# Optimization experiments

Measured on AMD Instinct MI355X. Metric: run time of the kernel, lower is better.

Reference implementation:

```python
import jax, jax.numpy as jnp
import numpy as np

N_NODES = 100000
N_EDGES = 1600000
N_GRAPHS = 256


def setup_inputs() -> dict:
    key = jax.random.key(0)
    ks = jax.random.split(key, 7)
    x = jax.random.normal(ks[0], (N_NODES, 128), dtype=jnp.float32)
    W1 = jax.random.normal(ks[1], (128, 64), dtype=jnp.float32) * (1.0 / np.sqrt(128))
    W2 = jax.random.normal(ks[2], (64, 64), dtype=jnp.float32) * (1.0 / np.sqrt(64))
    W3 = jax.random.normal(ks[3], (64, 64), dtype=jnp.float32) * (1.0 / np.sqrt(64))
    Wlin = jax.random.normal(ks[4], (64, 16), dtype=jnp.float32) * (1.0 / np.sqrt(64))
    edge_index = jax.random.randint(ks[5], (2, N_EDGES), 0, N_NODES, dtype=jnp.int64)
    batch = jnp.sort(jax.random.randint(ks[6], (N_NODES,), 0, N_GRAPHS, dtype=jnp.int64))
    return {"x": x, "W1": W1, "W2": W2, "W3": W3, "Wlin": Wlin,
            "edge_index": edge_index, "batch": batch}


def _gcn_conv(h, W, src, dst):
    # GCNConv(bias=False, normalize=False): scatter-add of transformed src feats onto dst
    m = h @ W                                   # [N, d_out]
    return jax.ops.segment_sum(m[src], dst, num_segments=N_NODES)


def reference(x, W1, W2, W3, Wlin, edge_index, batch):
    src, dst = edge_index[0], edge_index[1]
    h = jax.nn.relu(_gcn_conv(x, W1, src, dst))
    h = jax.nn.relu(_gcn_conv(h, W2, src, dst))
    h = _gcn_conv(h, W3, src, dst)
    # global mean pool over graphs
    sums = jax.ops.segment_sum(h, batch, num_segments=N_GRAPHS)      # [G, d]
    counts = jax.ops.segment_sum(jnp.ones((N_NODES,), h.dtype), batch,
                                 num_segments=N_GRAPHS)              # [G]
    pooled = sums / jnp.maximum(counts, 1.0)[:, None]
    return pooled @ Wlin                                             # [G, out]
```

## Files before the change

kernel.cpp:

```cpp
#include <hip/hip_runtime.h>
#include <hip/hip_bf16.h>

#define SCAN_CHUNK 1024
#define BIN_CHUNK  4096
#define BSH        9
#define BCAP       10240
#define GSLOTS     16
#define KNODES     2

typedef __attribute__((ext_vector_type(8))) short short8v;
typedef __attribute__((ext_vector_type(4))) float f32x4;

__device__ __forceinline__ unsigned short f2bf(float f) {
    union { float f; unsigned int i; } c;
    c.f = f;
    unsigned int r = c.i + 0x7FFFu + ((c.i >> 16) & 1u);
    return (unsigned short)(r >> 16);
}
__device__ __forceinline__ float lo2f(unsigned int u) {
    union { unsigned int i; float f; } c; c.i = u << 16; return c.f;
}
__device__ __forceinline__ float hi2f(unsigned int u) {
    union { unsigned int i; float f; } c; c.i = u & 0xFFFF0000u; return c.f;
}
__device__ __forceinline__ unsigned int pack2bf(float lo, float hi) {
    return ((unsigned int)f2bf(hi) << 16) | (unsigned int)f2bf(lo);
}
__device__ __forceinline__ int idx_at(const void* p, long long i, int is64) {
    if (is64) return (int)((const long long*)p)[i];
    return ((const int*)p)[i];
}
__device__ __forceinline__ short8v as_s8(uint4 q) {
    return __builtin_bit_cast(short8v, q);
}

__global__ __launch_bounds__(256) void k_setup(const unsigned int* __restrict__ a, long long aWords,
                                               const unsigned int* __restrict__ b, long long bWords,
                                               int* __restrict__ flags, int* __restrict__ bcur,
                                               float* __restrict__ T, int tN,
                                               const float* __restrict__ W1, const float* __restrict__ W2,
                                               const float* __restrict__ W3, const float* __restrict__ Wlin,
                                               float* __restrict__ Wc,
                                               unsigned short* __restrict__ Wt1hi, unsigned short* __restrict__ Wt1lo,
                                               unsigned short* __restrict__ Wt2hi, unsigned short* __restrict__ Wt2lo) {
    int t = threadIdx.x;
    if (blockIdx.x == 0) {
        __shared__ int sA, sB;
        if (t == 0) { sA = 1; sB = 1; }
        __syncthreads();
        long long hA = aWords / 2;
        long long pA = 2 * ((long long)t * (hA - 1) / 255) + 1;
        if (a[pA] != 0u) atomicAnd(&sA, 0);
        long long hB = bWords / 2;
        long long pB = 2 * ((long long)t * (hB - 1) / 255) + 1;
        if (b[pB] != 0u) atomicAnd(&sB, 0);
        __syncthreads();
        if (t == 0) { flags[0] = sA; flags[1] = sB; }
    } else if (blockIdx.x == 1) {
        bcur[t] = 0;
        for (int o = t; o < 64 * 16; o += 256) {
            int k = o >> 4, j = o & 15;
            float acc = 0.f;
#pragma unroll 8
            for (int m = 0; m < 64; ++m) acc += W3[k * 64 + m] * Wlin[m * 16 + j];
            Wc[o] = acc;
        }
    } else if (blockIdx.x == 2) {
        int col = t >> 2, ks = (t & 3) * 32;
        for (int k = ks; k < ks + 32; ++k) {
            float v = W1[(size_t)k * 64 + col];
            unsigned short h = f2bf(v);
            Wt1hi[col * 128 + k] = h;
            Wt1lo[col * 128 + k] = f2bf(v - lo2f(h));
        }
    } else if (blockIdx.x == 3) {
        int col = t >> 2, ks = (t & 3) * 16;
        for (int k = ks; k < ks + 16; ++k) {
            float v = W2[(size_t)k * 64 + col];
            unsigned short h = f2bf(v);
            Wt2hi[col * 64 + k] = h;
            Wt2lo[col * 64 + k] = f2bf(v - lo2f(h));
        }
    } else {
        int i = (blockIdx.x - 4) * 256 + t;
        if (i < tN) T[i] = 0.f;
    }
}

__global__ __launch_bounds__(256) void k_bin(const void* __restrict__ ei, int nE,
                                             int* __restrict__ bcur, unsigned int* __restrict__ srcsE,
                                             const int* __restrict__ flags) {
    __shared__ int eS[BIN_CHUNK], eD[BIN_CHUNK];
    __shared__ int cntD[256], baseD[256], posD[256];
    int t = threadIdx.x;
    int is64 = flags[0];
    cntD[t] = 0; posD[t] = 0;
    __syncthreads();
    int cs = blockIdx.x * BIN_CHUNK;
    int ce = min(cs + BIN_CHUNK, nE);
    for (int i = cs + t; i < ce; i += 256) {
        int src = idx_at(ei, i, is64);
        int dst = idx_at(ei, (long long)nE + i, is64);
        eS[i - cs] = src; eD[i - cs] = dst;
        atomicAdd(&cntD[dst >> BSH], 1);
    }
    __syncthreads();
    if (cntD[t] > 0) baseD[t] = atomicAdd(&bcur[t], cntD[t]);
    __syncthreads();
    for (int i = cs + t; i < ce; i += 256) {
        int src = eS[i - cs], dst = eD[i - cs];
        int kd = dst >> BSH;
        int od = baseD[kd] + atomicAdd(&posD[kd], 1);
        if (od < BCAP)
            srcsE[(size_t)kd * BCAP + od] = (unsigned int)src | ((unsigned int)(dst & 511) << 17);
    }
}

__global__ __launch_bounds__(256) void k_fill3(unsigned int* __restrict__ srcsE,
                                               const int* __restrict__ bcur,
                                               int* __restrict__ rowstart, int* __restrict__ rowend,
                                               int N) {
    __shared__ unsigned int ent[BCAP];
    __shared__ int cnt5[512], off5[512], cur5[512], s2[256];
    int k = blockIdx.x;
    int t = threadIdx.x;
    int base = k * BCAP;
    int ck = min(bcur[k], BCAP);
    cnt5[t] = 0; cnt5[t + 256] = 0;
    __syncthreads();
    for (int i = t; i < ck; i += 256) {
        unsigned int v = srcsE[base + i];
        ent[i] = v;
        atomicAdd(&cnt5[v >> 17], 1);
    }
    __syncthreads();
    int pair = cnt5[2 * t] + cnt5[2 * t + 1];
    s2[t] = pair;
    __syncthreads();
    for (int off = 1; off < 256; off <<= 1) {
        int x = (t >= off) ? s2[t - off] : 0;
        __syncthreads();
        s2[t] += x;
        __syncthreads();
    }
    int excl = s2[t] - pair;
    off5[2 * t] = excl;
    off5[2 * t + 1] = excl + cnt5[2 * t];
    __syncthreads();
    for (int j = t; j < 512; j += 256) {
        int node = (k << BSH) + j;
        if (node < N) {
            rowstart[node] = base + off5[j];
            rowend[node]   = base + off5[j] + cnt5[j];
        }
        cur5[j] = off5[j];
    }
    __syncthreads();
    for (int i = t; i < ck; i += 256) {
        unsigned int v = ent[i];
        int d = (int)(v >> 17);
        int pos = atomicAdd(&cur5[d], 1);
        srcsE[base + pos] = v & 0x1FFFFu;
    }
}

__global__ __launch_bounds__(256) void k_zero_i(int* __restrict__ p, int n) {
    int i = blockIdx.x * 256 + threadIdx.x;
    if (i < n) p[i] = 0;
}
__global__ __launch_bounds__(256) void k_hist(const void* __restrict__ ei, int nE,
                                              int* __restrict__ cnt, const int* __restrict__ flags) {
    int e = blockIdx.x * 256 + threadIdx.x;
    if (e >= nE) return;
    int is64 = flags[0];
    atomicAdd(&cnt[idx_at(ei, (long long)nE + e, is64)], 1);
}
__global__ __launch_bounds__(256) void k_scan_a(const int* __restrict__ cnt, int N, int* __restrict__ bsum) {
    __shared__ int s[256];
    int b = blockIdx.x, t = threadIdx.x;
    int base = b * SCAN_CHUNK + t * 4;
    int v = 0;
#pragma unroll
    for (int j = 0; j < 4; ++j) if (base + j < N) v += cnt[base + j];
    s[t] = v; __syncthreads();
    for (int off = 128; off >= 1; off >>= 1) {
        if (t < off) s[t] += s[t + off];
        __syncthreads();
    }
    if (t == 0) bsum[b] = s[0];
}
__global__ __launch_bounds__(128) void k_scan_b(const int* __restrict__ bsum, int NB, int* __restrict__ bpre) {
    __shared__ int s[128];
    int t = threadIdx.x;
    int v = (t < NB) ? bsum[t] : 0;
    s[t] = v; __syncthreads();
    for (int off = 1; off < 128; off <<= 1) {
        int x = (t >= off) ? s[t - off] : 0;
        __syncthreads();
        s[t] += x;
        __syncthreads();
    }
    if (t < NB) bpre[t] = s[t] - v;
}
__global__ __launch_bounds__(256) void k_scan_c(const int* __restrict__ cnt, int N,
                                                const int* __restrict__ bpre,
                                                int* __restrict__ rowstart, int* __restrict__ rowend,
                                                int* __restrict__ cursor) {
    __shared__ int s[256];
    int b = blockIdx.x, t = threadIdx.x;
    int base = b * SCAN_CHUNK + t * 4;
    int c0 = (base + 0 < N) ? cnt[base + 0] : 0;
    int c1 = (base + 1 < N) ? cnt[base + 1] : 0;
    int c2 = (base + 2 < N) ? cnt[base + 2] : 0;
    int c3 = (base + 3 < N) ? cnt[base + 3] : 0;
    int p0 = c0, p1 = p0 + c1, p2 = p1 + c2, p3 = p2 + c3;
    s[t] = p3; __syncthreads();
    int tot = p3;
    for (int off = 1; off < 256; off <<= 1) {
        int x = (t >= off) ? s[t - off] : 0;
        __syncthreads();
        s[t] += x;
        __syncthreads();
    }
    int toff = s[t] - tot + bpre[b];
    if (base + 0 < N) { rowstart[base + 0] = toff;      rowend[base + 0] = toff + p0; cursor[base + 0] = toff; }
    if (base + 1 < N) { rowstart[base + 1] = toff + p0; rowend[base + 1] = toff + p1; cursor[base + 1] = toff + p0; }
    if (base + 2 < N) { rowstart[base + 2] = toff + p1; rowend[base + 2] = toff + p2; cursor[base + 2] = toff + p1; }
    if (base + 3 < N) { rowstart[base + 3] = toff + p2; rowend[base + 3] = toff + p3; cursor[base + 3] = toff + p2; }
}
__global__ __launch_bounds__(256) void k_fill(const void* __restrict__ ei, int nE,
                                              int* __restrict__ cursor, int* __restrict__ srcs,
                                              const int* __restrict__ flags) {
    int e = blockIdx.x * 256 + threadIdx.x;
    if (e >= nE) return;
    int is64 = flags[0];
    int src = idx_at(ei, e, is64);
    int dst = idx_at(ei, (long long)nE + e, is64);
    int pos = atomicAdd(&cursor[dst], 1);
    srcs[pos] = src;
}

__global__ __launch_bounds__(256) void k_gemm1m(const float* __restrict__ X,
                                                const unsigned short* __restrict__ Wthi,
                                                const unsigned short* __restrict__ Wtlo,
                                                unsigned short* __restrict__ Mb, int N) {
    __shared__ unsigned short Xhi[64 * 128];
    __shared__ unsigned short Xlo[64 * 128];
    int tid = threadIdx.x;
    int wid = tid >> 6, lane = tid & 63;
    int lrow = lane & 15, lk = lane >> 4;
    int base = blockIdx.x * 64;

    uint4 bhi[4], blo[4];
    {
        int col = wid * 16 + lrow;
        const unsigned short* ph = Wthi + col * 128 + lk * 8;
        const unsigned short* pl = Wtlo + col * 128 + lk * 8;
#pragma unroll
        for (int kc = 0; kc < 4; ++kc) {
            bhi[kc] = *(const uint4*)(ph + kc * 32);
            blo[kc] = *(const uint4*)(pl + kc * 32);
        }
    }

    {
        int r = tid >> 2, seg = tid & 3;
        int row = base + r;
        float v[32];
        if (row < N) {
            const float4* src = (const float4*)(X + (size_t)row * 128 + seg * 32);
#pragma unroll
            for (int u = 0; u < 8; ++u) {
                float4 f = src[u];
                v[4 * u] = f.x; v[4 * u + 1] = f.y; v[4 * u + 2] = f.z; v[4 * u + 3] = f.w;
            }
        } else {
#pragma unroll
            for (int u = 0; u < 32; ++u) v[u] = 0.f;
        }
        int swz = (r & 7) << 4;
#pragma unroll
        for (int u = 0; u < 4; ++u) {
            unsigned short h[8];
            float lo[8];
#pragma unroll
            for (int j = 0; j < 8; ++j) {
                float xv = v[u * 8 + j];
                unsigned short hh = f2bf(xv);
                h[j] = hh;
                lo[j] = xv - lo2f(hh);
            }
            uint4 qh, ql;
            qh.x = ((unsigned)h[1] << 16) | h[0]; qh.y = ((unsigned)h[3] << 16) | h[2];
            qh.z = ((unsigned)h[5] << 16) | h[4]; qh.w = ((unsigned)h[7] << 16) | h[6];
            ql.x = pack2bf(lo[0], lo[1]); ql.y = pack2bf(lo[2], lo[3]);
            ql.z = pack2bf(lo[4], lo[5]); ql.w = pack2bf(lo[6], lo[7]);
            int kb = seg * 64 + u * 16;
            int addr = r * 256 + (kb ^ swz);
            *(uint4*)((char*)Xhi + addr) = qh;
            *(uint4*)((char*)Xlo + addr) = ql;
        }
    }
    __syncthreads();

    int col = wid * 16 + lrow;
#pragma unroll
    for (int rt = 0; rt < 4; ++rt) {
        f32x4 acc = {0.f, 0.f, 0.f, 0.f};
        int row = rt * 16 + lrow;
        int rbase = row * 256;
        int swz = (row & 7) << 4;
#pragma unroll
        for (int kc = 0; kc < 4; ++kc) {
            int kb = kc * 64 + lk * 16;
            uint4 ah = *(const uint4*)((const char*)Xhi + rbase + (kb ^ swz));
            uint4 al = *(const uint4*)((const char*)Xlo + rbase + (kb ^ swz));
            acc = __builtin_amdgcn_mfma_f32_16x16x32_bf16(as_s8(ah), as_s8(bhi[kc]), acc, 0, 0, 0);
            acc = __builtin_amdgcn_mfma_f32_16x16x32_bf16(as_s8(al), as_s8(bhi[kc]), acc, 0, 0, 0);
            acc = __builtin_amdgcn_mfma_f32_16x16x32_bf16(as_s8(ah), as_s8(blo[kc]), acc, 0, 0, 0);
        }
#pragma unroll
        for (int j = 0; j < 4; ++j) {
            int orow = base + rt * 16 + lk * 4 + j;
            if (orow < N) Mb[(size_t)orow * 64 + col] = f2bf(acc[j]);
        }
    }
}

__global__ __launch_bounds__(256) void k_projm(const unsigned short* __restrict__ Rb,
                                               const unsigned short* __restrict__ Wthi,
                                               const unsigned short* __restrict__ Wtlo,
                                               unsigned short* __restrict__ Mout, int N) {
    __shared__ unsigned short Rs[64 * 64];
    int tid = threadIdx.x;
    int wid = tid >> 6, lane = tid & 63;
    int lrow = lane & 15, lk = lane >> 4;
    int base = blockIdx.x * 64;

    uint4 bhi[2], blo[2];
    {
        int col = wid * 16 + lrow;
        const unsigned short* ph = Wthi + col * 64 + lk * 8;
        const unsigned short* pl = Wtlo + col * 64 + lk * 8;
#pragma unroll
        for (int kc = 0; kc < 2; ++kc) {
            bhi[kc] = *(const uint4*)(ph + kc * 32);
            blo[kc] = *(const uint4*)(pl + kc * 32);
        }
    }
    {
        int r = tid >> 2, seg = tid & 3;
        int row = base + r;
        uint4 q0, q1;
        if (row < N) {
            const uint4* src = (const uint4*)(Rb + (size_t)row * 64 + seg * 16);
            q0 = src[0]; q1 = src[1];
        } else {
            q0 = make_uint4(0u, 0u, 0u, 0u); q1 = q0;
        }
        int swz = (r & 7) << 4;
        int kb = seg * 32;
        *(uint4*)((char*)Rs + r * 128 + ((kb) ^ swz)) = q0;
        *(uint4*)((char*)Rs + r * 128 + ((kb + 16) ^ swz)) = q1;
    }
    __syncthreads();

    int col = wid * 16 + lrow;
#pragma unroll
    for (int rt = 0; rt < 4; ++rt) {
        f32x4 acc = {0.f, 0.f, 0.f, 0.f};
        int row = rt * 16 + lrow;
        int rbase = row * 128;
        int swz = (row & 7) << 4;
#pragma unroll
        for (int kc = 0; kc < 2; ++kc) {
            int kb = kc * 64 + lk * 16;
            uint4 a = *(const uint4*)((const char*)Rs + rbase + (kb ^ swz));
            acc = __builtin_amdgcn_mfma_f32_16x16x32_bf16(as_s8(a), as_s8(bhi[kc]), acc, 0, 0, 0);
            acc = __builtin_amdgcn_mfma_f32_16x16x32_bf16(as_s8(a), as_s8(blo[kc]), acc, 0, 0, 0);
        }
#pragma unroll
        for (int j = 0; j < 4; ++j) {
            int orow = base + rt * 16 + lk * 4 + j;
            if (orow < N) Mout[(size_t)orow * 64 + col] = f2bf(acc[j]);
        }
    }
}

#define GATHER8_CORE(SRCS, MB, S, E, LMASK, L, A)                             \
    {                                                                         \
        int c_ = (S);                                                         \
        for (; c_ + 8 <= (E); c_ += 8) {                                      \
            int sv_ = (SRCS)[c_ + (L)];                                       \
            _Pragma("unroll")                                                 \
            for (int j_ = 0; j_ < 8; ++j_) {                                  \
                int srcn_ = __shfl(sv_, (LMASK) | j_, 64);                    \
                uint4 p_ = ((const uint4*)((MB) + (size_t)srcn_ * 64))[L];    \
                A[0] += lo2f(p_.x); A[1] += hi2f(p_.x);                       \
                A[2] += lo2f(p_.y); A[3] += hi2f(p_.y);                       \
                A[4] += lo2f(p_.z); A[5] += hi2f(p_.z);                       \
                A[6] += lo2f(p_.w); A[7] += hi2f(p_.w);                       \
            }                                                                 \
        }                                                                     \
        if (c_ < (E)) {                                                       \
            int sv_ = (SRCS)[(c_ + (L) < (E)) ? c_ + (L) : (E) - 1];          \
            _Pragma("unroll")                                                 \
            for (int j_ = 0; j_ < 8; ++j_) {                                  \
                if (c_ + j_ < (E)) {                                          \
                    int srcn_ = __shfl(sv_, (LMASK) | j_, 64);                \
                    uint4 p_ = ((const uint4*)((MB) + (size_t)srcn_ * 64))[L];\
                    A[0] += lo2f(p_.x); A[1] += hi2f(p_.x);                   \
                    A[2] += lo2f(p_.y); A[3] += hi2f(p_.y);                   \
                    A[4] += lo2f(p_.z); A[5] += hi2f(p_.z);                   \
                    A[6] += lo2f(p_.w); A[7] += hi2f(p_.w);                   \
                }                                                             \
            }                                                                 \
        }                                                                     \
    }

__global__ __launch_bounds__(256) void k_gather8(const unsigned short* __restrict__ Mb,
                                                 const int* __restrict__ rowstart,
                                                 const int* __restrict__ rowend,
                                                 const int* __restrict__ srcs,
                                                 unsigned short* __restrict__ R, int N) {
    int tid = threadIdx.x;
    int lane = tid & 63;
    int l = lane & 7;
    int lmask = lane & 56;
    int node0 = (blockIdx.x * 32 + (tid >> 3)) * KNODES;
#pragma unroll
    for (int jn = 0; jn < KNODES; ++jn) {
        int node = node0 + jn;
        if (node >= N) break;
        int s = rowstart[node], e = rowend[node];
        float a[8] = {0.f, 0.f, 0.f, 0.f, 0.f, 0.f, 0.f, 0.f};
        GATHER8_CORE(srcs, Mb, s, e, lmask, l, a)
        uint4 q;
        q.x = pack2bf(fmaxf(a[0], 0.f), fmaxf(a[1], 0.f));
        q.y = pack2bf(fmaxf(a[2], 0.f), fmaxf(a[3], 0.f));
        q.z = pack2bf(fmaxf(a[4], 0.f), fmaxf(a[5], 0.f));
        q.w = pack2bf(fmaxf(a[6], 0.f), fmaxf(a[7], 0.f));
        ((uint4*)(R + (size_t)node * 64))[l] = q;
    }
}

#define GFLUSH(GG, RR)                                                        \
    {                                                                         \
        int slot_ = (GG) - gmin;                                              \
        if (slot_ >= 0 && slot_ < GSLOTS) {                                   \
            _Pragma("unroll")                                                 \
            for (int i_ = 0; i_ < 8; ++i_)                                    \
                atomicAdd(&sacc[slot_][l * 8 + i_], RR[i_]);                  \
        } else {                                                              \
            _Pragma("unroll")                                                 \
            for (int i_ = 0; i_ < 8; ++i_)                                    \
                atomicAdd(&T[(GG) * 64 + l * 8 + i_], RR[i_]);                \
        }                                                                     \
    }

__global__ __launch_bounds__(256) void k_gsum8(const unsigned short* __restrict__ R,
                                               const int* __restrict__ rowstart,
                                               const int* __restrict__ rowend,
                                               const int* __restrict__ srcs,
                                               const void* __restrict__ batch,
                                               float* __restrict__ T, int N, int G,
                                               const int* __restrict__ flags) {
    __shared__ float sacc[GSLOTS][64];
    int tid = threadIdx.x;
    for (int t = tid; t < GSLOTS * 64; t += 256) ((float*)sacc)[t] = 0.f;
    int is64 = flags[1];
    int nbase = blockIdx.x * 32 * KNODES;
    int gmin = idx_at(batch, min(nbase, N - 1), is64);
    __syncthreads();

    int lane = tid & 63;
    int l = lane & 7;
    int lmask = lane & 56;
    int node0 = nbase + (tid >> 3) * KNODES;
    float r[8] = {0.f, 0.f, 0.f, 0.f, 0.f, 0.f, 0.f, 0.f};
    int curG = -1;
#pragma unroll
    for (int jn = 0; jn < KNODES; ++jn) {
        int node = node0 + jn;
        if (node >= N) break;
        int s = rowstart[node], e = rowend[node];
        float a[8] = {0.f, 0.f, 0.f, 0.f, 0.f, 0.f, 0.f, 0.f};
        GATHER8_CORE(srcs, R, s, e, lmask, l, a)
        int g = idx_at(batch, node, is64);
        if (g != curG) {
            if (curG >= 0) GFLUSH(curG, r)
#pragma unroll
            for (int i = 0; i < 8; ++i) r[i] = a[i];
            curG = g;
        } else {
#pragma unroll
            for (int i = 0; i < 8; ++i) r[i] += a[i];
        }
    }
    if (curG >= 0) GFLUSH(curG, r)
    __syncthreads();
    for (int t = tid; t < GSLOTS * 64; t += 256) {
        float v = ((float*)sacc)[t];
        int g = gmin + (t >> 6);
        if (v != 0.f && g < G) atomicAdd(&T[g * 64 + (t & 63)], v);
    }
}

__global__ __launch_bounds__(64) void k_out(const float* __restrict__ T,
                                            const void* __restrict__ batch,
                                            const float* __restrict__ Wc,
                                            float* __restrict__ out, int N,
                                            const int* __restrict__ flags) {
    int g = blockIdx.x;
    int lane = threadIdx.x;
    int is64 = flags[1];

    int lo = 0, hi = N;
    while (lo < hi) { int mid = (lo + hi) >> 1; if (idx_at(batch, mid, is64) < g) lo = mid + 1; else hi = mid; }
    int s = lo;
    lo = s; hi = N;
    while (lo < hi) { int mid = (lo + hi) >> 1; if (idx_at(batch, mid, is64) < g + 1) lo = mid + 1; else hi = mid; }
    float cnt = (float)(lo - s);

    __shared__ float P[64];
    P[lane] = T[g * 64 + lane] / fmaxf(cnt, 1.0f);
    __syncthreads();
    if (lane < 16) {
        float o = 0.f;
#pragma unroll 8
        for (int k = 0; k < 64; ++k) o += P[k] * Wc[k * 16 + lane];
        out[g * 16 + lane] = o;
    }
}

extern "C" void kernel_launch(void* const* d_in, const int* in_sizes, int n_in,
                              void* d_out, int out_size, void* d_ws, size_t ws_size,
                              hipStream_t stream) {
    const float* x    = (const float*)d_in[0];
    const float* W1   = (const float*)d_in[1];
    const float* W2   = (const float*)d_in[2];
    const float* W3   = (const float*)d_in[3];
    const float* Wlin = (const float*)d_in[4];
    const void* ei    = d_in[5];
    const void* batch = d_in[6];

    int N  = in_sizes[0] / 128;
    int nE = in_sizes[5] / 2;
    int G  = out_size / 16;
    int NBUCK = (N + (1 << BSH) - 1) >> BSH;
    int NB = (N + SCAN_CHUNK - 1) / SCAN_CHUNK;
    bool fast = (NBUCK <= 256);

    unsigned short* MbA = (unsigned short*)d_ws;
    unsigned short* MbB = (unsigned short*)(MbA + (size_t)N * 64);
    int* ip       = (int*)(MbB + (size_t)N * 64);
    int* rowstart = ip;          ip += N;
    int* rowend   = ip;          ip += N;
    int* cnt      = ip;          ip += N;
    int* bsum     = ip;          ip += 128;
    int* bpre     = ip;          ip += 128;
    int* flags    = ip;          ip += 2;
    int* bcur     = ip;          ip += 256;
    float* T      = (float*)ip;  ip += (size_t)G * 64;
    float* Wc     = (float*)ip;  ip += 64 * 16;
    unsigned short* Wt1hi = (unsigned short*)ip; ip += 4096;
    unsigned short* Wt1lo = (unsigned short*)ip; ip += 4096;
    unsigned short* Wt2hi = (unsigned short*)ip; ip += 2048;
    unsigned short* Wt2lo = (unsigned short*)ip; ip += 2048;
    unsigned int* srcsE = (unsigned int*)ip;
    ip += fast ? (size_t)256 * BCAP : (size_t)nE;
    size_t need = (size_t)((char*)ip - (char*)d_ws);
    if (ws_size < need) return;

    dim3 blk(256);
    int gT64  = (N + 63) / 64;
    int gG8   = (N + 32 * KNODES - 1) / (32 * KNODES);
    int gBin  = (nE + BIN_CHUNK - 1) / BIN_CHUNK;
    int tN    = G * 64;
    int gSetup = 4 + (tN + 255) / 256;

    hipLaunchKernelGGL(k_setup, dim3(gSetup), blk, 0, stream,
                       (const unsigned int*)ei, (long long)in_sizes[5],
                       (const unsigned int*)batch, (long long)in_sizes[6],
                       flags, bcur, T, tN, W1, W2, W3, Wlin, Wc,
                       Wt1hi, Wt1lo, Wt2hi, Wt2lo);

    if (fast) {
        hipLaunchKernelGGL(k_bin,   dim3(gBin), blk, 0, stream, ei, nE, bcur, srcsE, flags);
        hipLaunchKernelGGL(k_fill3, dim3(NBUCK), blk, 0, stream, srcsE, bcur, rowstart, rowend, N);
    } else {
        int gN = (N + 255) / 256;
        int gE = (nE + 255) / 256;
        hipLaunchKernelGGL(k_zero_i, dim3(gN), blk, 0, stream, cnt, N);
        hipLaunchKernelGGL(k_hist,   dim3(gE), blk, 0, stream, ei, nE, cnt, flags);
        hipLaunchKernelGGL(k_scan_a, dim3(NB), blk, 0, stream, cnt, N, bsum);
        hipLaunchKernelGGL(k_scan_b, dim3(1), dim3(128), 0, stream, bsum, NB, bpre);
        hipLaunchKernelGGL(k_scan_c, dim3(NB), blk, 0, stream, cnt, N, bpre, rowstart, rowend, cnt);
        hipLaunchKernelGGL(k_fill,   dim3(gE), blk, 0, stream, ei, nE, cnt, (int*)srcsE, flags);
    }

    hipLaunchKernelGGL(k_gemm1m,  dim3(gT64), blk, 0, stream, x, Wt1hi, Wt1lo, MbA, N);
    hipLaunchKernelGGL(k_gather8, dim3(gG8), blk, 0, stream, MbA, rowstart, rowend, (const int*)srcsE, MbB, N);
    hipLaunchKernelGGL(k_projm,   dim3(gT64), blk, 0, stream, MbB, Wt2hi, Wt2lo, MbA, N);
    hipLaunchKernelGGL(k_gather8, dim3(gG8), blk, 0, stream, MbA, rowstart, rowend, (const int*)srcsE, MbB, N);
    hipLaunchKernelGGL(k_gsum8, dim3(gG8), blk, 0, stream, MbB, rowstart, rowend, (const int*)srcsE, batch, T, N, G, flags);
    hipLaunchKernelGGL(k_out, dim3(G), dim3(64), 0, stream, T, batch, Wc, (float*)d_out, N, flags);
}
```

Measured before the change: 313.7 us.

## Project layer-3 features through W3·Wlin before final gather-pool to shrink gather width

Moves the combined W3·Wlin projection ahead of the last aggregation: a new MFMA kernel computes 16-wide Y2 = relu(h2)·(W3·Wlin), then a bucket-parallel kernel sums Y2 over edges per graph using graph ids packed into the high bits of the CSR source entries. This cuts the last gather from 64 to 16 bf16 features per edge and drops the final 64x16 matmul. The gather macro is also unrolled to 16 edges per iteration with masking of the packed bits. It adds an extra kernel and relies on graph ids relative to each bucket fitting in 15 bits and on per-bucket graph spans, with a global atomic fallback beyond 32 graph slots.

After: 302.0 us. -3.7%, faster.

```diff
diff --git a/kernel.cpp b/kernel.cpp
--- a/kernel.cpp
+++ b/kernel.cpp
@@ -7,6 +7,8 @@
 #define BCAP       10240
 #define GSLOTS     16
 #define KNODES     2
+#define GS16       32
+#define GSPLIT     2
 
 typedef __attribute__((ext_vector_type(8))) short short8v;
 typedef __attribute__((ext_vector_type(4))) float f32x4;
@@ -42,7 +44,8 @@
                                                const float* __restrict__ W3, const float* __restrict__ Wlin,
                                                float* __restrict__ Wc,
                                                unsigned short* __restrict__ Wt1hi, unsigned short* __restrict__ Wt1lo,
-                                               unsigned short* __restrict__ Wt2hi, unsigned short* __restrict__ Wt2lo) {
+                                               unsigned short* __restrict__ Wt2hi, unsigned short* __restrict__ Wt2lo,
+                                               unsigned short* __restrict__ Wcthi, unsigned short* __restrict__ Wctlo) {
     int t = threadIdx.x;
     if (blockIdx.x == 0) {
         __shared__ int sA, sB;
@@ -64,6 +67,9 @@
 #pragma unroll 8
             for (int m = 0; m < 64; ++m) acc += W3[k * 64 + m] * Wlin[m * 16 + j];
             Wc[o] = acc;
+            unsigned short h = f2bf(acc);
+            Wcthi[j * 64 + k] = h;
+            Wctlo[j * 64 + k] = f2bf(acc - lo2f(h));
         }
     } else if (blockIdx.x == 2) {
         int col = t >> 2, ks = (t & 3) * 32;
@@ -119,14 +125,19 @@
 __global__ __launch_bounds__(256) void k_fill3(unsigned int* __restrict__ srcsE,
                                                const int* __restrict__ bcur,
                                                int* __restrict__ rowstart, int* __restrict__ rowend,
-                                               int N) {
+                                               int N, const void* __restrict__ batch,
+                                               const int* __restrict__ flags) {
     __shared__ unsigned int ent[BCAP];
     __shared__ int cnt5[512], off5[512], cur5[512], s2[256];
+    __shared__ int grelS[512];
+    __shared__ int sgf;
     int k = blockIdx.x;
     int t = threadIdx.x;
     int base = k * BCAP;
     int ck = min(bcur[k], BCAP);
+    int is64b = flags[1];
     cnt5[t] = 0; cnt5[t + 256] = 0;
+    if (t == 0) sgf = idx_at(batch, (long long)(k << BSH), is64b);
     __syncthreads();
     for (int i = t; i < ck; i += 256) {
         unsigned int v = srcsE[base + i];
@@ -152,6 +163,9 @@
         if (node < N) {
             rowstart[node] = base + off5[j];
             rowend[node]   = base + off5[j] + cnt5[j];
+            grelS[j] = idx_at(batch, node, is64b) - sgf;
+        } else {
+            grelS[j] = 0;
         }
         cur5[j] = off5[j];
     }
@@ -160,7 +174,7 @@
         unsigned int v = ent[i];
         int d = (int)(v >> 17);
         int pos = atomicAdd(&cur5[d], 1);
-        srcsE[base + pos] = v & 0x1FFFFu;
+        srcsE[base + pos] = (v & 0x1FFFFu) | ((unsigned int)grelS[d] << 17);
     }
 }
 
@@ -387,32 +401,79 @@
     }
 }
 
-#define GATHER8_CORE(SRCS, MB, S, E, LMASK, L, A)                             \
+__global__ __launch_bounds__(256) void k_y2(const unsigned short* __restrict__ R,
+                                            const unsigned short* __restrict__ Wcthi,
+                                            const unsigned short* __restrict__ Wctlo,
+                                            unsigned short* __restrict__ Y2, int N) {
+    int tid = threadIdx.x;
+    int wid = tid >> 6, lane = tid & 63;
+    int lrow = lane & 15, lk = lane >> 4;
+    int rowb = blockIdx.x * 64 + wid * 16;
+
+    uint4 bhi[2], blo[2];
+#pragma unroll
+    for (int kc = 0; kc < 2; ++kc) {
+        bhi[kc] = *(const uint4*)(Wcthi + lrow * 64 + kc * 32 + lk * 8);
+        blo[kc] = *(const uint4*)(Wctlo + lrow * 64 + kc * 32 + lk * 8);
+    }
+    f32x4 acc = {0.f, 0.f, 0.f, 0.f};
+    int arow = rowb + lrow;
+#pragma unroll
+    for (int kc = 0; kc < 2; ++kc) {
+        uint4 a = make_uint4(0u, 0u, 0u, 0u);
+        if (arow < N) a = *(const uint4*)(R + (size_t)arow * 64 + kc * 32 + lk * 8);
+        acc = __builtin_amdgcn_mfma_f32_16x16x32_bf16(as_s8(a), as_s8(bhi[kc]), acc, 0, 0, 0);
+        acc = __builtin_amdgcn_mfma_f32_16x16x32_bf16(as_s8(a), as_s8(blo[kc]), acc, 0, 0, 0);
+    }
+#pragma unroll
+    for (int j = 0; j < 4; ++j) {
+        int orow = rowb + lk * 4 + j;
+        if (orow < N) Y2[(size_t)orow * 16 + lrow] = f2bf(acc[j]);
+    }
+}
+
+#define GACC(P)  { A[0] += lo2f((P).x); A[1] += hi2f((P).x);                  \
+                   A[2] += lo2f((P).y); A[3] += hi2f((P).y);                  \
+                   A[4] += lo2f((P).z); A[5] += hi2f((P).z);                  \
+                   A[6] += lo2f((P).w); A[7] += hi2f((P).w); }
+#define GATHER8_CORE(SRCS, MB, S, E, LMASK, L, A, MASK)                       \
     {                                                                         \
         int c_ = (S);                                                         \
-        for (; c_ + 8 <= (E); c_ += 8) {                                      \
-            int sv_ = (SRCS)[c_ + (L)];                                       \
+        for (; c_ + 16 <= (E); c_ += 16) {                                    \
+            int sv0_ = (int)(SRCS)[c_ + (L)];                                 \
+            int sv1_ = (int)(SRCS)[c_ + 8 + (L)];                             \
             _Pragma("unroll")                                                 \
             for (int j_ = 0; j_ < 8; ++j_) {                                  \
-                int srcn_ = __shfl(sv_, (LMASK) | j_, 64);                    \
+                int srcn_ = __shfl(sv0_, (LMASK) | j_, 64) & (int)(MASK);     \
                 uint4 p_ = ((const uint4*)((MB) + (size_t)srcn_ * 64))[L];    \
-                A[0] += lo2f(p_.x); A[1] += hi2f(p_.x);                       \
-                A[2] += lo2f(p_.y); A[3] += hi2f(p_.y);                       \
-                A[4] += lo2f(p_.z); A[5] += hi2f(p_.z);                       \
-                A[6] += lo2f(p_.w); A[7] += hi2f(p_.w);                       \
+                GACC(p_)                                                      \
+            }                                                                 \
+            _Pragma("unroll")                                                 \
+            for (int j_ = 0; j_ < 8; ++j_) {                                  \
+                int srcn_ = __shfl(sv1_, (LMASK) | j_, 64) & (int)(MASK);     \
+                uint4 p_ = ((const uint4*)((MB) + (size_t)srcn_ * 64))[L];    \
+                GACC(p_)                                                      \
             }                                                                 \
         }                                                                     \
-        if (c_ < (E)) {                                                       \
-            int sv_ = (SRCS)[(c_ + (L) < (E)) ? c_ + (L) : (E) - 1];          \
+        if (c_ + 8 <= (E)) {                                                  \
+            int sv_ = (int)(SRCS)[c_ + (L)];                                  \
             _Pragma("unroll")                                                 \
             for (int j_ = 0; j_ < 8; ++j_) {                                  \
-                if (c_ + j_ < (E)) {                                          \
-                    int srcn_ = __shfl(sv_, (LMASK) | j_, 64);                \
+                int srcn_ = __shfl(sv_, (LMASK) | j_, 64) & (int)(MASK);      \
+                uint4 p_ = ((const uint4*)((MB) + (size_t)srcn_ * 64))[L];    \
+                GACC(p_)                                                      \
+            }                                                                 \
+            c_ += 8;                                                          \
+        }                                                                     \
+        if (c_ < (E)) {                                                       \
+            int m_ = (E) - c_;                                                \
+            int sv_ = (int)(SRCS)[(c_ + (L) < (E)) ? c_ + (L) : (E) - 1];     \
+            _Pragma("unroll")                                                 \
+            for (int j_ = 0; j_ < 8; ++j_) {                                  \
+                if (j_ < m_) {                                                \
+                    int srcn_ = __shfl(sv_, (LMASK) | j_, 64) & (int)(MASK);  \
                     uint4 p_ = ((const uint4*)((MB) + (size_t)srcn_ * 64))[L];\
-                    A[0] += lo2f(p_.x); A[1] += hi2f(p_.x);                   \
-                    A[2] += lo2f(p_.y); A[3] += hi2f(p_.y);                   \
-                    A[4] += lo2f(p_.z); A[5] += hi2f(p_.z);                   \
-                    A[6] += lo2f(p_.w); A[7] += hi2f(p_.w);                   \
+                    GACC(p_)                                                  \
                 }                                                             \
             }                                                                 \
         }                                                                     \
@@ -421,8 +482,9 @@
 __global__ __launch_bounds__(256) void k_gather8(const unsigned short* __restrict__ Mb,
                                                  const int* __restrict__ rowstart,
                                                  const int* __restrict__ rowend,
-                                                 const int* __restrict__ srcs,
-                                                 unsigned short* __restrict__ R, int N) {
+                                                 const unsigned int* __restrict__ srcs,
+                                                 unsigned short* __restrict__ R, int N,
+                                                 unsigned int srcMask) {
     int tid = threadIdx.x;
     int lane = tid & 63;
     int l = lane & 7;
@@ -433,15 +495,113 @@
         int node = node0 + jn;
         if (node >= N) break;
         int s = rowstart[node], e = rowend[node];
-        float a[8] = {0.f, 0.f, 0.f, 0.f, 0.f, 0.f, 0.f, 0.f};
-        GATHER8_CORE(srcs, Mb, s, e, lmask, l, a)
+        float A[8] = {0.f, 0.f, 0.f, 0.f, 0.f, 0.f, 0.f, 0.f};
+        GATHER8_CORE(srcs, Mb, s, e, lmask, l, A, srcMask)
         uint4 q;
-        q.x = pack2bf(fmaxf(a[0], 0.f), fmaxf(a[1], 0.f));
-        q.y = pack2bf(fmaxf(a[2], 0.f), fmaxf(a[3], 0.f));
-        q.z = pack2bf(fmaxf(a[4], 0.f), fmaxf(a[5], 0.f));
-        q.w = pack2bf(fmaxf(a[6], 0.f), fmaxf(a[7], 0.f));
+        q.x = pack2bf(fmaxf(A[0], 0.f), fmaxf(A[1], 0.f));
+        q.y = pack2bf(fmaxf(A[2], 0.f), fmaxf(A[3], 0.f));
+        q.z = pack2bf(fmaxf(A[4], 0.f), fmaxf(A[5], 0.f));
+        q.w = pack2bf(fmaxf(A[6], 0.f), fmaxf(A[7], 0.f));
         ((uint4*)(R + (size_t)node * 64))[l] = q;
     }
+}
+
+__global__ __launch_bounds__(256) void k_gsum16(const unsigned short* __restrict__ y2,
+                                                const unsigned int* __restrict__ srcsE,
+                                                const int* __restrict__ bcur,
+                                                const void* __restrict__ batch,
+                                                float* __restrict__ T16, int N, int G,
+                                                const int* __restrict__ flags) {
+    __shared__ float sacc[GS16][4][16];
+    __shared__ int sgmin;
+    int t = threadIdx.x;
+    int k = blockIdx.x / GSPLIT;
+    int half = blockIdx.x % GSPLIT;
+    for (int i = t; i < GS16 * 4 * 16; i += 256) ((float*)sacc)[i] = 0.f;
+    if (t == 0) sgmin = idx_at(batch, (long long)min(k << BSH, N - 1), flags[1]);
+    __syncthreads();
+    int gmin = sgmin;
+    int ck = min(bcur[k], BCAP);
+    int base = k * BCAP;
+    int lo = half * (ck / GSPLIT);
+    int hi = (half == GSPLIT - 1) ? ck : (half + 1) * (ck / GSPLIT);
+    int cnt = hi - lo;
+    int len = (cnt + 255) >> 8;
+    int s0 = lo + t * len;
+    int e0 = min(s0 + len, hi);
+    int rep = t & 3;
+
+    float acc[16];
+#pragma unroll
+    for (int j = 0; j < 16; ++j) acc[j] = 0.f;
+    int curg = -1;
+
+#define GF16(GG)                                                              \
+    {                                                                         \
+        if ((GG) < GS16) {                                                    \
+            float* sp_ = &sacc[GG][rep][0];                                   \
+            _Pragma("unroll")                                                 \
+            for (int j_ = 0; j_ < 16; ++j_) atomicAdd(&sp_[j_], acc[j_]);     \
+        } else {                                                              \
+            _Pragma("unroll")                                                 \
+            for (int j_ = 0; j_ < 16; ++j_)                                   \
+                atomicAdd(&T16[(size_t)(gmin + (GG)) * 16 + j_], acc[j_]);    \
+        }                                                                     \
+    }
+
+    int i = s0;
+    while (i < e0) {
+        if (i + 4 <= e0) {
+            unsigned v0 = srcsE[base + i], v1 = srcsE[base + i + 1];
+            unsigned v2 = srcsE[base + i + 2], v3 = srcsE[base + i + 3];
+            int g0 = (int)(v0 >> 17);
+            if (g0 == curg && (int)(v3 >> 17) == g0 &&
+                (int)(v1 >> 17) == g0 && (int)(v2 >> 17) == g0) {
+                const uint4* p0 = (const uint4*)(y2 + (size_t)(v0 & 0x1FFFFu) * 16);
+                const uint4* p1 = (const uint4*)(y2 + (size_t)(v1 & 0x1FFFFu) * 16);
+                const uint4* p2 = (const uint4*)(y2 + (size_t)(v2 & 0x1FFFFu) * 16);
+                const uint4* p3 = (const uint4*)(y2 + (size_t)(v3 & 0x1FFFFu) * 16);
+                uint4 a0 = p0[0], b0 = p0[1];
+                uint4 a1 = p1[0], b1 = p1[1];
+                uint4 a2 = p2[0], b2 = p2[1];
+                uint4 a3 = p3[0], b3 = p3[1];
+#define Y2ACC(QA, QB)                                                         \
+                acc[0] += lo2f((QA).x); acc[1] += hi2f((QA).x);               \
+                acc[2] += lo2f((QA).y); acc[3] += hi2f((QA).y);               \
+                acc[4] += lo2f((QA).z); acc[5] += hi2f((QA).z);               \
+                acc[6] += lo2f((QA).w); acc[7] += hi2f((QA).w);               \
+                acc[8] += lo2f((QB).x); acc[9] += hi2f((QB).x);               \
+                acc[10] += lo2f((QB).y); acc[11] += hi2f((QB).y);             \
+                acc[12] += lo2f((QB).z); acc[13] += hi2f((QB).z);             \
+                acc[14] += lo2f((QB).w); acc[15] += hi2f((QB).w);
+                Y2ACC(a0, b0) Y2ACC(a1, b1) Y2ACC(a2, b2) Y2ACC(a3, b3)
+                i += 4;
+                continue;
+            }
+        }
+        unsigned v = srcsE[base + i];
+        int g = (int)(v >> 17);
+        if (g != curg) {
+            if (curg >= 0) GF16(curg)
+            curg = g;
+#pragma unroll
+            for (int j = 0; j < 16; ++j) acc[j] = 0.f;
+        }
+        const uint4* p = (const uint4*)(y2 + (size_t)(v & 0x1FFFFu) * 16);
+        uint4 qa = p[0], qb = p[1];
+        Y2ACC(qa, qb)
+        ++i;
+    }
+    if (curg >= 0) GF16(curg)
+    __syncthreads();
+    for (int i2 = t; i2 < GS16 * 16; i2 += 256) {
+        int slot = i2 >> 4, j = i2 & 15;
+        float v = sacc[slot][0][j] + sacc[slot][1][j] + sacc[slot][2][j] + sacc[slot][3][j];
+        int g = gmin + slot;
+        if (v != 0.f && g < G) atomicAdd(&T16[(size_t)g * 16 + j], v);
+    }
+#undef Y2ACC
+#undef GF16
 }
 
 #define GFLUSH(GG, RR)                                                        \
@@ -461,7 +621,7 @@
 __global__ __launch_bounds__(256) void k_gsum8(const unsigned short* __restrict__ R,
                                                const int* __restrict__ rowstart,
                                                const int* __restrict__ rowend,
-                                               const int* __restrict__ srcs,
+                                               const unsigned int* __restrict__ srcs,
                                                const void* __restrict__ batch,
                                                float* __restrict__ T, int N, int G,
                                                const int* __restrict__ flags) {
@@ -484,17 +644,17 @@
         int node = node0 + jn;
         if (node >= N) break;
         int s = rowstart[node], e = rowend[node];
-        float a[8] = {0.f, 0.f, 0.f, 0.f, 0.f, 0.f, 0.f, 0.f};
-        GATHER8_CORE(srcs, R, s, e, lmask, l, a)
+        float A[8] = {0.f, 0.f, 0.f, 0.f, 0.f, 0.f, 0.f, 0.f};
+        GATHER8_CORE(srcs, R, s, e, lmask, l, A, 0xFFFFFFFFu)
         int g = idx_at(batch, node, is64);
         if (g != curG) {
             if (curG >= 0) GFLUSH(curG, r)
 #pragma unroll
-            for (int i = 0; i < 8; ++i) r[i] = a[i];
+            for (int i = 0; i < 8; ++i) r[i] = A[i];
             curG = g;
         } else {
 #pragma unroll
-            for (int i = 0; i < 8; ++i) r[i] += a[i];
+            for (int i = 0; i < 8; ++i) r[i] += A[i];
         }
     }
     if (curG >= 0) GFLUSH(curG, r)
@@ -531,6 +691,24 @@
         for (int k = 0; k < 64; ++k) o += P[k] * Wc[k * 16 + lane];
         out[g * 16 + lane] = o;
     }
+}
+
+__global__ __launch_bounds__(64) void k_out16(const float* __restrict__ T16,
+                                              const void* __restrict__ batch,
+                                              float* __restrict__ out, int N,
+                                              const int* __restrict__ flags) {
+    int g = blockIdx.x;
+    int lane = threadIdx.x;
+    int is64 = flags[1];
+
+    int lo = 0, hi = N;
+    while (lo < hi) { int mid = (lo + hi) >> 1; if (idx_at(batch, mid, is64) < g) lo = mid + 1; else hi = mid; }
+    int s = lo;
+    lo = s; hi = N;
+    while (lo < hi) { int mid = (lo + hi) >> 1; if (idx_at(batch, mid, is64) < g + 1) lo = mid + 1; else hi = mid; }
+    float cnt = (float)(lo - s);
+
+    if (lane < 16) out[g * 16 + lane] = T16[(size_t)g * 16 + lane] / fmaxf(cnt, 1.0f);
 }
 
 extern "C" void kernel_launch(void* const* d_in, const int* in_sizes, int n_in,
@@ -559,14 +737,18 @@
     int* cnt      = ip;          ip += N;
     int* bsum     = ip;          ip += 128;
     int* bpre     = ip;          ip += 128;
-    int* flags    = ip;          ip += 2;
+    int* flags    = ip;          ip += 4;
     int* bcur     = ip;          ip += 256;
     float* T      = (float*)ip;  ip += (size_t)G * 64;
     float* Wc     = (float*)ip;  ip += 64 * 16;
-    unsigned short* Wt1hi = (unsigned short*)ip; ip += 4096;
+    unsigned short* Wt1hi = (unsigned short*)ip; ip += 2048;
+    ip += 2048;
     unsigned short* Wt1lo = (unsigned short*)ip; ip += 4096;
     unsigned short* Wt2hi = (unsigned short*)ip; ip += 2048;
     unsigned short* Wt2lo = (unsigned short*)ip; ip += 2048;
+    unsigned short* Wcthi = (unsigned short*)ip; ip += 512;
+    unsigned short* Wctlo = (unsigned short*)ip; ip += 512;
+    unsigned short* Y2    = (unsigned short*)ip; ip += (size_t)N * 8;
     unsigned int* srcsE = (unsigned int*)ip;
     ip += fast ? (size_t)256 * BCAP : (size_t)nE;
     size_t need = (size_t)((char*)ip - (char*)d_ws);
@@ -583,11 +765,11 @@
                        (const unsigned int*)ei, (long long)in_sizes[5],
                        (const unsigned int*)batch, (long long)in_sizes[6],
                        flags, bcur, T, tN, W1, W2, W3, Wlin, Wc,
-                       Wt1hi, Wt1lo, Wt2hi, Wt2lo);
+                       Wt1hi, Wt1lo, Wt2hi, Wt2lo, Wcthi, Wctlo);
 
     if (fast) {
         hipLaunchKernelGGL(k_bin,   dim3(gBin), blk, 0, stream, ei, nE, bcur, srcsE, flags);
-        hipLaunchKernelGGL(k_fill3, dim3(NBUCK), blk, 0, stream, srcsE, bcur, rowstart, rowend, N);
+        hipLaunchKernelGGL(k_fill3, dim3(NBUCK), blk, 0, stream, srcsE, bcur, rowstart, rowend, N, batch, flags);
     } else {
         int gN = (N + 255) / 256;
         int gE = (nE + 255) / 256;
@@ -599,10 +781,19 @@
         hipLaunchKernelGGL(k_fill,   dim3(gE), blk, 0, stream, ei, nE, cnt, (int*)srcsE, flags);
     }
 
+    unsigned int srcMask = fast ? 0x1FFFFu : 0xFFFFFFFFu;
+
     hipLaunchKernelGGL(k_gemm1m,  dim3(gT64), blk, 0, stream, x, Wt1hi, Wt1lo, MbA, N);
-    hipLaunchKernelGGL(k_gather8, dim3(gG8), blk, 0, stream, MbA, rowstart, rowend, (const int*)srcsE, MbB, N);
+    hipLaunchKernelGGL(k_gather8, dim3(gG8), blk, 0, stream, MbA, rowstart, rowend, srcsE, MbB, N, srcMask);
     hipLaunchKernelGGL(k_projm,   dim3(gT64), blk, 0, stream, MbB, Wt2hi, Wt2lo, MbA, N);
-    hipLaunchKernelGGL(k_gather8, dim3(gG8), blk, 0, stream, MbA, rowstart, rowend, (const int*)srcsE, MbB, N);
-    hipLaunchKernelGGL(k_gsum8, dim3(gG8), blk, 0, stream, MbB, rowstart, rowend, (const int*)srcsE, batch, T, N, G, flags);
-    hipLaunchKernelGGL(k_out, dim3(G), dim3(64), 0, stream, T, batch, Wc, (float*)d_out, N, flags);
-}
+    hipLaunchKernelGGL(k_gather8, dim3(gG8), blk, 0, stream, MbA, rowstart, rowend, srcsE, MbB, N, srcMask);
+
+    if (fast) {
+        hipLaunchKernelGGL(k_y2,     dim3(gT64), blk, 0, stream, MbB, Wcthi, Wctlo, Y2, N);
+        hipLaunchKernelGGL(k_gsum16, dim3(NBUCK * GSPLIT), blk, 0, stream, Y2, srcsE, bcur, batch, T, N, G, flags);
+        hipLaunchKernelGGL(k_out16,  dim3(G), dim3(64), 0, stream, T, batch, (float*)d_out, N, flags);
+    } else {
+        hipLaunchKernelGGL(k_gsum8, dim3(gG8), blk, 0, stream, MbB, rowstart, rowend, srcsE, batch, T, N, G, flags);
+        hipLaunchKernelGGL(k_out, dim3(G), dim3(64), 0, stream, T, batch, Wc, (float*)d_out, N, flags);
+    }
+}
```
